# Performance work log

Hardware: AMD Instinct MI355X
Metric: run time of the kernel (lower is better)

## Reference

```python
import jax, jax.numpy as jnp
import numpy as np

TOP_K = 2
SCALE = 1.0  # score_scale_factor

def setup_inputs() -> dict:
    key = jax.random.key(0)
    ks = jax.random.split(key, 8)
    T, D, E, F = 4096, 1024, 8, 4096
    return {
        "hidden_states": jax.random.normal(ks[0], (T, D), jnp.float32),
        "gw1": jax.random.normal(ks[1], (D, D // 4), jnp.float32) * 0.02,
        "gb1": jnp.zeros((D // 4,), jnp.float32),
        "gw2": jax.random.normal(ks[2], (D // 4, D // 16), jnp.float32) * 0.02,
        "gb2": jnp.zeros((D // 16,), jnp.float32),
        "gw3": jax.random.normal(ks[3], (D // 16, E), jnp.float32) * 0.02,
        "w1": jax.random.normal(ks[4], (E, D, F), jnp.float32) * 0.02,
        "b1": jnp.zeros((E, F), jnp.float32),
        "w2": jax.random.normal(ks[5], (E, F, D), jnp.float32) * 0.02,
        "b2": jnp.zeros((E, D), jnp.float32),
    }

def reference(hidden_states, gw1, gb1, gw2, gb2, gw3, w1, b1, w2, b2):
    h = hidden_states                              # [T, D]
    g = jax.nn.relu(h @ gw1 + gb1)
    g = jax.nn.relu(g @ gw2 + gb2)
    router_logits = g @ gw3                        # [T, E]
    probs = jax.nn.softmax(router_logits.astype(jnp.float32), axis=-1)
    top_w, top_i = jax.lax.top_k(probs, TOP_K)     # [T, k]
    top_w = top_w / jnp.sum(top_w, axis=-1, keepdims=True)
    top_w = top_w.astype(h.dtype)
    T, E = router_logits.shape
    # combine weights: scatter normalized top-k weights into dense [T, E]
    cw = jnp.zeros((T, E), h.dtype).at[jnp.arange(T)[:, None], top_i].add(top_w)
    out = jnp.zeros_like(h)
    for e in range(E):  # small fixed expert count
        y = jax.nn.gelu(h @ w1[e] + b1[e]) @ w2[e] + b2[e]
        out = out + y * (cw[:, e:e + 1] * SCALE)
    return out, router_logits
```

## Files before the change

### kernel.cpp

```cpp
#include <hip/hip_runtime.h>
#include <stdint.h>

#define T_  4096
#define D_  1024
#define E_  8
#define F_  4096
#define H1_ 256
#define H2_ 64
#define SCALE_ 1.0f
#define NROW_ (2 * T_)
#define NT2_ 40

typedef unsigned short ushort_t;
typedef unsigned int   uint32;
typedef __attribute__((ext_vector_type(8))) short  short8;
typedef __attribute__((ext_vector_type(4))) float  f32x4;
typedef __attribute__((ext_vector_type(8))) unsigned short us8;

#define BARRIER() do { asm volatile("" ::: "memory"); __builtin_amdgcn_s_barrier(); asm volatile("" ::: "memory"); } while (0)
#define WAITVM(N) asm volatile("s_waitcnt vmcnt(" #N ")" ::: "memory")

__device__ __forceinline__ ushort_t f2bf(float f) {
  uint32 u = __float_as_uint(f);
  u += 0x7FFFu + ((u >> 16) & 1u);
  return (ushort_t)(u >> 16);
}
__device__ __forceinline__ float gelu_tanh(float x) {
  float u = 0.7978845608028654f * (x + 0.044715f * x * x * x);
  float e = __expf(2.0f * u);
  return 0.5f * x * (1.0f + (1.0f - 2.0f / (e + 1.0f)));
}
__device__ __forceinline__ void gll16(const void* gptr, void* lptr) {
  void* g = const_cast<void*>(gptr);
  __builtin_amdgcn_global_load_lds((__attribute__((address_space(1))) void*)g,
                                   (__attribute__((address_space(3))) void*)lptr,
                                   16, 0, 0);
}

__device__ __forceinline__ void stage8(const ushort_t* a0, const ushort_t* a1,
                                       const ushort_t* b0, const ushort_t* b1,
                                       short8 (*An)[16][64], short8 (*Bn)[16][64], int w) {
  gll16(a0,      &An[0][w * 2 + 0][0]);
  gll16(a0 + 32, &An[1][w * 2 + 0][0]);
  gll16(a1,      &An[0][w * 2 + 1][0]);
  gll16(a1 + 32, &An[1][w * 2 + 1][0]);
  gll16(b0,      &Bn[0][w * 2 + 0][0]);
  gll16(b0 + 32, &Bn[1][w * 2 + 0][0]);
  gll16(b1,      &Bn[0][w * 2 + 1][0]);
  gll16(b1 + 32, &Bn[1][w * 2 + 1][0]);
}

__device__ __forceinline__ void mfma_step64(const short8 (*Ac)[16][64], const short8 (*Bc)[16][64],
                                            int wr, int wc, int lane, f32x4 acc[8][4]) {
#pragma unroll
  for (int ks = 0; ks < 2; ++ks) {
    short8 af[8], bf4[4];
#pragma unroll
    for (int i = 0; i < 8; ++i) af[i] = Ac[ks][wr * 8 + i][lane];
#pragma unroll
    for (int j = 0; j < 4; ++j) bf4[j] = Bc[ks][wc * 4 + j][lane];
#pragma unroll
    for (int i = 0; i < 8; ++i)
#pragma unroll
      for (int j = 0; j < 4; ++j)
        acc[i][j] = __builtin_amdgcn_mfma_f32_16x16x32_bf16(af[i], bf4[j], acc[i][j], 0, 0, 0);
  }
}

__global__ void k_cvt_h(const float* __restrict__ h, ushort_t* __restrict__ hb) {
  int i = (blockIdx.x * 256 + threadIdx.x) * 8;
  float4 a = *(const float4*)(h + i);
  float4 b = *(const float4*)(h + i + 4);
  short8 v;
  v[0] = (short)f2bf(a.x); v[1] = (short)f2bf(a.y);
  v[2] = (short)f2bf(a.z); v[3] = (short)f2bf(a.w);
  v[4] = (short)f2bf(b.x); v[5] = (short)f2bf(b.y);
  v[6] = (short)f2bf(b.z); v[7] = (short)f2bf(b.w);
  *(short8*)(hb + i) = v;
}

__global__ void k_transpose_bf16(const float* __restrict__ in, ushort_t* __restrict__ out,
                                 int R, int C) {
  __shared__ float ltf[64][65];
  const size_t per = (size_t)R * C;
  const float* src = in + per * blockIdx.z;
  ushort_t* dst = out + per * blockIdx.z;
  int r0 = blockIdx.x * 64, c0 = blockIdx.y * 64;
  int tid = threadIdx.x;
  int cg = (tid & 15) * 4;
  int rr = tid >> 4;
#pragma unroll
  for (int rb = 0; rb < 64; rb += 16) {
    int r = rb + rr;
    float4 v = *(const float4*)(src + (size_t)(r0 + r) * C + c0 + cg);
    ltf[r][cg + 0] = v.x; ltf[r][cg + 1] = v.y;
    ltf[r][cg + 2] = v.z; ltf[r][cg + 3] = v.w;
  }
  __syncthreads();
  int c = tid >> 2, rch = (tid & 3) * 16;
  ushort_t tmp[16];
#pragma unroll
  for (int i = 0; i < 16; ++i) tmp[i] = f2bf(ltf[rch + i][c]);
  ushort_t* dp = dst + (size_t)(c0 + c) * R + r0 + rch;
  *(us8*)dp = *(const us8*)&tmp[0];
  *(us8*)(dp + 8) = *(const us8*)&tmp[8];
}

__global__ void k_router1(const float* __restrict__ h, const float* __restrict__ gw1,
                          double* __restrict__ p1) {
  __shared__ float sA[16][65];
  __shared__ float sB[16][65];
  int tx = threadIdx.x, ty = threadIdx.y;
  int tid = ty * 16 + tx;
  int m0 = blockIdx.y * 64, n0 = blockIdx.x * 64;
  int kc = blockIdx.z;
  double acc[4][4] = {};
  for (int k0 = kc * 256; k0 < kc * 256 + 256; k0 += 16) {
    {
      int m = tid & 63, kq = tid >> 6;
      float4 v = *(const float4*)(h + (size_t)(m0 + m) * D_ + k0 + kq * 4);
      sA[kq*4+0][m] = v.x; sA[kq*4+1][m] = v.y; sA[kq*4+2][m] = v.z; sA[kq*4+3][m] = v.w;
    }
    {
      int k = tid >> 4, nq = tid & 15;
      float4 v = *(const float4*)(gw1 + (size_t)(k0 + k) * H1_ + n0 + nq * 4);
      sB[k][nq*4+0] = v.x; sB[k][nq*4+1] = v.y; sB[k][nq*4+2] = v.z; sB[k][nq*4+3] = v.w;
    }
    __syncthreads();
#pragma unroll
    for (int k = 0; k < 16; ++k) {
      float a[4], b[4];
#pragma unroll
      for (int i = 0; i < 4; ++i) a[i] = sA[k][ty + i * 16];
#pragma unroll
      for (int j = 0; j < 4; ++j) b[j] = sB[k][tx * 4 + j];
#pragma unroll
      for (int i = 0; i < 4; ++i)
#pragma unroll
        for (int j = 0; j < 4; ++j)
          acc[i][j] += (double)a[i] * (double)b[j];
    }
    __syncthreads();
  }
  double* pd = p1 + (size_t)kc * T_ * H1_;
  for (int i = 0; i < 4; ++i)
    for (int j = 0; j < 4; ++j) {
      int m = m0 + ty + i * 16, n = n0 + tx * 4 + j;
      pd[(size_t)m * H1_ + n] = acc[i][j];
    }
}

__global__ void k_router23(const double* __restrict__ p1, const float* __restrict__ gb1,
                           const float* __restrict__ gw2, const float* __restrict__ gb2,
                           const float* __restrict__ gw3,
                           float* __restrict__ logits_out, int* __restrict__ tokExp,
                           float* __restrict__ tokW, int* __restrict__ counts) {
  __shared__ double sG1[4][256];
  __shared__ double sG2[4][64];
  __shared__ double sL[4][8];
  int lane = threadIdx.x & 63, wv = threadIdx.x >> 6;
  int t = blockIdx.x * 4 + wv;
  const size_t TH = (size_t)T_ * H1_;
  const double* gp = p1 + (size_t)t * H1_ + lane * 4;
  double s0 = 0, s1 = 0, s2 = 0, s3 = 0;
#pragma unroll
  for (int kc = 0; kc < 4; ++kc) {
    double2 va = *(const double2*)(gp + kc * TH);
    double2 vb = *(const double2*)(gp + kc * TH + 2);
    s0 += va.x; s1 += va.y; s2 += vb.x; s3 += vb.y;
  }
  int hbase = lane * 4;
  s0 += (double)gb1[hbase + 0]; s1 += (double)gb1[hbase + 1];
  s2 += (double)gb1[hbase + 2]; s3 += (double)gb1[hbase + 3];
  sG1[wv][hbase + 0] = s0 > 0.0 ? s0 : 0.0;
  sG1[wv][hbase + 1] = s1 > 0.0 ? s1 : 0.0;
  sG1[wv][hbase + 2] = s2 > 0.0 ? s2 : 0.0;
  sG1[wv][hbase + 3] = s3 > 0.0 ? s3 : 0.0;
  __syncthreads();
  double acc = (double)gb2[lane];
  for (int k = 0; k < H1_; ++k)
    acc += sG1[wv][k] * (double)gw2[k * H2_ + lane];
  sG2[wv][lane] = acc > 0.0 ? acc : 0.0;
  __syncthreads();
  if (lane < 8) {
    double l = 0.0;
    for (int j = 0; j < H2_; ++j) l += sG2[wv][j] * (double)gw3[j * E_ + lane];
    sL[wv][lane] = l;
    logits_out[(size_t)t * E_ + lane] = (float)l;
  }
  __syncthreads();
  if (lane == 0) {
    double best = -1e300, second = -1e300; int bi = 0, si = 0;
    for (int e = 0; e < E_; ++e) {
      double l = sL[wv][e];
      if (l > best)        { second = best; si = bi; best = l; bi = e; }
      else if (l > second) { second = l; si = e; }
    }
    double w0 = 1.0 / (1.0 + exp(second - best));
    tokExp[t*2]   = bi; tokExp[t*2+1] = si;
    tokW[t*2]     = (float)w0;
    tokW[t*2+1]   = (float)(1.0 - w0);
    atomicAdd(&counts[bi], 1);
    atomicAdd(&counts[si], 1);
  }
}

__global__ void k_assign(const int* __restrict__ tokExp, const int* __restrict__ counts,
                         int* cursor, int* __restrict__ list, int* __restrict__ rowOf,
                         int* __restrict__ tileTab) {
  int offs[E_];
  int s = 0;
#pragma unroll
  for (int e = 0; e < E_; ++e) { offs[e] = s; s += counts[e]; }
  if (blockIdx.x == 0 && threadIdx.x == 0) {
    int nt = 0;
    for (int e = 0; e < E_; ++e) {
      int cnt = counts[e];
      for (int m = 0; m * 256 < cnt; ++m) {
        tileTab[nt*3+0] = e;
        tileTab[nt*3+1] = offs[e] + m * 256;
        tileTab[nt*3+2] = (cnt - m * 256) < 256 ? (cnt - m * 256) : 256;
        ++nt;
      }
    }
    for (; nt < NT2_; ++nt) tileTab[nt*3+0] = -1;
  }
  int t = blockIdx.x * 256 + threadIdx.x;
  for (int k = 0; k < 2; ++k) {
    int e = tokExp[t*2+k];
    int pos = atomicAdd(&cursor[e], 1);
    int row = offs[e] + pos;
    list[row] = t;
    rowOf[t*2+k] = row;
  }
}

__global__ __launch_bounds__(512, 1) void k_moe_ffn1(
    const ushort_t* __restrict__ hb, const ushort_t* __restrict__ w1t,
    const float* __restrict__ b1, ushort_t* __restrict__ act,
    const int* __restrict__ list, const int* __restrict__ tileTab, int* q) {
  __shared__ short8 lA[2][2][16][64];
  __shared__ short8 lB[2][2][16][64];
  __shared__ int sIdx;
  int tid = threadIdx.x, w = tid >> 6, lane = tid & 63;
  int m16 = lane & 15, kq = lane >> 4;
  int wr = w >> 2, wc = w & 3;
  int quad = lane >> 4, cn = lane & 15;
  for (;;) {
    __syncthreads();
    if (tid == 0) sIdx = atomicAdd(q, 1);
    __syncthreads();
    int idx = sIdx;
    if (idx >= NT2_ * 16) return;
    int ti = idx >> 4, nb = idx & 15;
    int e = tileTab[ti*3+0];
    if (e < 0) continue;
    int rowStart = tileTab[ti*3+1];
    int cntTile  = tileTab[ti*3+2];
    int nBase = nb * 256;
    const ushort_t* B = w1t + (size_t)e * F_ * D_;
    int gr0 = rowStart + w * 32 + m16;
    int gr1 = gr0 + 16;
    int t0 = list[min(gr0, NROW_ - 1)];
    int t1 = list[min(gr1, NROW_ - 1)];
    const ushort_t* aS0 = hb + (size_t)t0 * D_ + kq * 8;
    const ushort_t* aS1 = hb + (size_t)t1 * D_ + kq * 8;
    const ushort_t* bS0 = B + (size_t)(nBase + w * 32 + m16) * D_ + kq * 8;
    const ushort_t* bS1 = bS0 + (size_t)16 * D_;
    f32x4 acc[8][4] = {};
    stage8(aS0, aS1, bS0, bS1, lA[0], lB[0], w);
    const int NSTEP = D_ / 64;
    for (int t = 0; t < NSTEP - 1; ++t) {
      int k0 = (t + 1) * 64;
      stage8(aS0 + k0, aS1 + k0, bS0 + k0, bS1 + k0, lA[(t + 1) & 1], lB[(t + 1) & 1], w);
      WAITVM(8);
      BARRIER();
      mfma_step64(lA[t & 1], lB[t & 1], wr, wc, lane, acc);
      BARRIER();
    }
    WAITVM(0);
    BARRIER();
    mfma_step64(lA[(NSTEP - 1) & 1], lB[(NSTEP - 1) & 1], wr, wc, lane, acc);
    const float* b1e = b1 + (size_t)e * F_;
    float bj[4];
#pragma unroll
    for (int j = 0; j < 4; ++j) bj[j] = b1e[nBase + wc * 64 + j * 16 + cn];
#pragma unroll
    for (int i = 0; i < 8; ++i) {
      int lrow = wr * 128 + i * 16 + quad * 4;
#pragma unroll
      for (int r = 0; r < 4; ++r) {
        if (lrow + r < cntTile) {
          size_t gr = (size_t)rowStart + lrow + r;
#pragma unroll
          for (int j = 0; j < 4; ++j) {
            int n = nBase + wc * 64 + j * 16 + cn;
            float x = acc[i][j][r] + bj[j];
            act[gr * F_ + n] = f2bf(gelu_tanh(x));
          }
        }
      }
    }
  }
}

__global__ __launch_bounds__(512, 1) void k_moe_ffn2(
    const ushort_t* __restrict__ act, const ushort_t* __restrict__ w2t,
    float* __restrict__ part, const int* __restrict__ tileTab, int* q, int KC) {
  __shared__ short8 lA[2][2][16][64];
  __shared__ short8 lB[2][2][16][64];
  __shared__ int sIdx;
  int tid = threadIdx.x, w = tid >> 6, lane = tid & 63;
  int m16 = lane & 15, kq = lane >> 4;
  int wr = w >> 2, wc = w & 3;
  int quad = lane >> 4, cn = lane & 15;
  const int ipt = 4 * KC;
  const int kcs = F_ / KC;
  const int NSTEP = kcs / 64;
  for (;;) {
    __syncthreads();
    if (tid == 0) sIdx = atomicAdd(q, 1);
    __syncthreads();
    int idx = sIdx;
    if (idx >= NT2_ * ipt) return;
    int ti = idx / ipt, sub = idx - ti * ipt;
    int nb = sub / KC, kc = sub - nb * KC;
    int e = tileTab[ti*3+0];
    if (e < 0) continue;
    int rowStart = tileTab[ti*3+1];
    int cntTile  = tileTab[ti*3+2];
    int nBase = nb * 256;
    int kBase = kc * kcs;
    const ushort_t* Bw = w2t + (size_t)e * D_ * F_;
    int gr0 = rowStart + w * 32 + m16;
    int gr1 = gr0 + 16;
    const ushort_t* aS0 = act + (size_t)min(gr0, NROW_ - 1) * F_ + kBase + kq * 8;
    const ushort_t* aS1 = act + (size_t)min(gr1, NROW_ - 1) * F_ + kBase + kq * 8;
    const ushort_t* bS0 = Bw + (size_t)(nBase + w * 32 + m16) * F_ + kBase + kq * 8;
    const ushort_t* bS1 = bS0 + (size_t)16 * F_;
    f32x4 acc[8][4] = {};
    stage8(aS0, aS1, bS0, bS1, lA[0], lB[0], w);
    for (int t = 0; t < NSTEP - 1; ++t) {
      int k0 = (t + 1) * 64;
      stage8(aS0 + k0, aS1 + k0, bS0 + k0, bS1 + k0, lA[(t + 1) & 1], lB[(t + 1) & 1], w);
      WAITVM(8);
      BARRIER();
      mfma_step64(lA[t & 1], lB[t & 1], wr, wc, lane, acc);
      BARRIER();
    }
    WAITVM(0);
    BARRIER();
    mfma_step64(lA[(NSTEP - 1) & 1], lB[(NSTEP - 1) & 1], wr, wc, lane, acc);
    float* pd = part + (size_t)kc * NROW_ * D_;
#pragma unroll
    for (int i = 0; i < 8; ++i) {
      int lrow = wr * 128 + i * 16 + quad * 4;
#pragma unroll
      for (int r = 0; r < 4; ++r) {
        if (lrow + r < cntTile) {
          size_t gr = (size_t)rowStart + lrow + r;
#pragma unroll
          for (int j = 0; j < 4; ++j) {
            int n = nBase + wc * 64 + j * 16 + cn;
            pd[gr * D_ + n] = acc[i][j][r];
          }
        }
      }
    }
  }
}

__global__ void k_combine(const float* __restrict__ part, const int* __restrict__ rowOf,
                          const int* __restrict__ tokExp, const float* __restrict__ tokW,
                          const float* __restrict__ b2, float* __restrict__ out, int KC) {
  int t = blockIdx.x;
  int rA = rowOf[t*2], rB = rowOf[t*2+1];
  int eA = tokExp[t*2], eB = tokExp[t*2+1];
  float wA = tokW[t*2] * SCALE_, wB = tokW[t*2+1] * SCALE_;
  int d = threadIdx.x * 4;
  const size_t P = (size_t)NROW_ * D_;
  float sax = 0, say = 0, saz = 0, saw = 0;
  float sbx = 0, sby = 0, sbz = 0, sbw = 0;
  for (int k = 0; k < KC; ++k) {
    float4 a = *(const float4*)(part + (size_t)k * P + (size_t)rA * D_ + d);
    float4 b = *(const float4*)(part + (size_t)k * P + (size_t)rB * D_ + d);
    sax += a.x; say += a.y; saz += a.z; saw += a.w;
    sbx += b.x; sby += b.y; sbz += b.z; sbw += b.w;
  }
  float4 ba = *(const float4*)(b2 + (size_t)eA * D_ + d);
  float4 bb = *(const float4*)(b2 + (size_t)eB * D_ + d);
  float4 o;
  o.x = wA * (sax + ba.x) + wB * (sbx + bb.x);
  o.y = wA * (say + ba.y) + wB * (sby + bb.y);
  o.z = wA * (saz + ba.z) + wB * (sbz + bb.z);
  o.w = wA * (saw + ba.w) + wB * (sbw + bb.w);
  *(float4*)(out + (size_t)t * D_ + d) = o;
}

extern "C" void kernel_launch(void* const* d_in, const int* in_sizes, int n_in,
                              void* d_out, int out_size, void* d_ws, size_t ws_size,
                              hipStream_t stream) {
  const float* h   = (const float*)d_in[0];
  const float* gw1 = (const float*)d_in[1];
  const float* gb1 = (const float*)d_in[2];
  const float* gw2 = (const float*)d_in[3];
  const float* gb2 = (const float*)d_in[4];
  const float* gw3 = (const float*)d_in[5];
  const float* w1  = (const float*)d_in[6];
  const float* b1  = (const float*)d_in[7];
  const float* w2  = (const float*)d_in[8];
  const float* b2  = (const float*)d_in[9];
  float* out    = (float*)d_out;
  float* logits = out + (size_t)T_ * D_;

  char* ws = (char*)d_ws;
  size_t o = 0;
  auto alloc = [&](size_t bytes) -> void* {
    o = (o + 255) & ~(size_t)255;
    void* p = ws + o;
    o += bytes;
    return p;
  };
  int*      counts  = (int*)alloc((2 * E_ + 2) * 4);
  int*      cursor  = counts + E_;
  int*      qq      = counts + 2 * E_;
  int*      tileTab = (int*)alloc((size_t)NT2_ * 3 * 4);
  int*      tokExp  = (int*)alloc((size_t)T_ * 2 * 4);
  float*    tokW    = (float*)alloc((size_t)T_ * 2 * 4);
  int*      list    = (int*)alloc((size_t)NROW_ * 4);
  int*      rowOf   = (int*)alloc((size_t)NROW_ * 4);
  ushort_t* hb      = (ushort_t*)alloc((size_t)T_ * D_ * 2);
  ushort_t* w2t     = (ushort_t*)alloc((size_t)E_ * D_ * F_ * 2);
  char*     bigA    = (char*)alloc((size_t)NROW_ * F_ * 2);
  double*   p1      = (double*)bigA;
  ushort_t* act     = (ushort_t*)bigA;
  size_t oAligned = (o + 255) & ~(size_t)255;
  size_t w1tBytes = (size_t)E_ * D_ * F_ * 2;
  int KC = (ws_size >= oAligned + (size_t)4 * NROW_ * D_ * 4) ? 4 : 2;
  size_t partBytes = (size_t)KC * NROW_ * D_ * 4;
  char*     bigB    = (char*)alloc(partBytes > w1tBytes ? partBytes : w1tBytes);
  ushort_t* w1t     = (ushort_t*)bigB;
  float*    part    = (float*)bigB;
  (void)in_sizes; (void)n_in; (void)out_size;

  hipMemsetAsync(counts, 0, (2 * E_ + 2) * 4, stream);
  k_cvt_h<<<T_ * D_ / 2048, 256, 0, stream>>>(h, hb);
  k_transpose_bf16<<<dim3(D_ / 64, F_ / 64, E_), 256, 0, stream>>>(w1, w1t, D_, F_);
  k_transpose_bf16<<<dim3(F_ / 64, D_ / 64, E_), 256, 0, stream>>>(w2, w2t, F_, D_);
  k_router1<<<dim3(H1_ / 64, T_ / 64, 4), dim3(16, 16), 0, stream>>>(h, gw1, p1);
  k_router23<<<T_ / 4, 256, 0, stream>>>(p1, gb1, gw2, gb2, gw3, logits, tokExp, tokW, counts);
  k_assign<<<T_ / 256, 256, 0, stream>>>(tokExp, counts, cursor, list, rowOf, tileTab);
  k_moe_ffn1<<<256, 512, 0, stream>>>(hb, w1t, b1, act, list, tileTab, qq + 0);
  k_moe_ffn2<<<256, 512, 0, stream>>>(act, w2t, part, tileTab, qq + 1, KC);
  k_combine<<<T_, 256, 0, stream>>>(part, rowOf, tokExp, tokW, b2, out, KC);
}
```

Baseline: 906.9 us.

## Shrink FFN GEMM tiles to 256x128 and use three-stage LDS pipeline

Both expert GEMM kernels change from 256x256 output tiles to 256x128, with a 4x2 wave grid in place of 2x4, and per-wave accumulators halve. The double-buffered LDS loop with two barriers per k-step becomes a triple-buffered ring with one barrier per step, so loads run two steps ahead of the MFMA work. The aim is more work items for load balance, lower register pressure and better latency hiding. The cost is less reuse of each A tile, since every row block is now loaded twice as often per output column.

```diff
diff --git a/kernel.cpp b/kernel.cpp
--- a/kernel.cpp
+++ b/kernel.cpp
@@ -37,30 +37,28 @@
                                    16, 0, 0);
 }
 
-__device__ __forceinline__ void stage8(const ushort_t* a0, const ushort_t* a1,
-                                       const ushort_t* b0, const ushort_t* b1,
-                                       short8 (*An)[16][64], short8 (*Bn)[16][64], int w) {
+__device__ __forceinline__ void stage6(const ushort_t* a0, const ushort_t* a1,
+                                       const ushort_t* b0,
+                                       short8 (*An)[16][64], short8 (*Bn)[8][64], int w) {
   gll16(a0,      &An[0][w * 2 + 0][0]);
   gll16(a0 + 32, &An[1][w * 2 + 0][0]);
   gll16(a1,      &An[0][w * 2 + 1][0]);
   gll16(a1 + 32, &An[1][w * 2 + 1][0]);
-  gll16(b0,      &Bn[0][w * 2 + 0][0]);
-  gll16(b0 + 32, &Bn[1][w * 2 + 0][0]);
-  gll16(b1,      &Bn[0][w * 2 + 1][0]);
-  gll16(b1 + 32, &Bn[1][w * 2 + 1][0]);
-}
-
-__device__ __forceinline__ void mfma_step64(const short8 (*Ac)[16][64], const short8 (*Bc)[16][64],
-                                            int wr, int wc, int lane, f32x4 acc[8][4]) {
+  gll16(b0,      &Bn[0][w][0]);
+  gll16(b0 + 32, &Bn[1][w][0]);
+}
+
+__device__ __forceinline__ void mfma_step32(const short8 (*Ac)[16][64], const short8 (*Bc)[8][64],
+                                            int wr, int wc, int lane, f32x4 acc[4][4]) {
 #pragma unroll
   for (int ks = 0; ks < 2; ++ks) {
-    short8 af[8], bf4[4];
-#pragma unroll
-    for (int i = 0; i < 8; ++i) af[i] = Ac[ks][wr * 8 + i][lane];
+    short8 af[4], bf4[4];
+#pragma unroll
+    for (int i = 0; i < 4; ++i) af[i] = Ac[ks][wr * 4 + i][lane];
 #pragma unroll
     for (int j = 0; j < 4; ++j) bf4[j] = Bc[ks][wc * 4 + j][lane];
 #pragma unroll
-    for (int i = 0; i < 8; ++i)
+    for (int i = 0; i < 4; ++i)
 #pragma unroll
       for (int j = 0; j < 4; ++j)
         acc[i][j] = __builtin_amdgcn_mfma_f32_16x16x32_bf16(af[i], bf4[j], acc[i][j], 0, 0, 0);
@@ -239,25 +237,25 @@
     const ushort_t* __restrict__ hb, const ushort_t* __restrict__ w1t,
     const float* __restrict__ b1, ushort_t* __restrict__ act,
     const int* __restrict__ list, const int* __restrict__ tileTab, int* q) {
-  __shared__ short8 lA[2][2][16][64];
-  __shared__ short8 lB[2][2][16][64];
+  __shared__ short8 lA[3][2][16][64];
+  __shared__ short8 lB[3][2][8][64];
   __shared__ int sIdx;
   int tid = threadIdx.x, w = tid >> 6, lane = tid & 63;
   int m16 = lane & 15, kq = lane >> 4;
-  int wr = w >> 2, wc = w & 3;
+  int wr = w >> 1, wc = w & 1;
   int quad = lane >> 4, cn = lane & 15;
   for (;;) {
     __syncthreads();
     if (tid == 0) sIdx = atomicAdd(q, 1);
     __syncthreads();
     int idx = sIdx;
-    if (idx >= NT2_ * 16) return;
-    int ti = idx >> 4, nb = idx & 15;
+    if (idx >= NT2_ * 32) return;
+    int ti = idx >> 5, nb = idx & 31;
     int e = tileTab[ti*3+0];
     if (e < 0) continue;
     int rowStart = tileTab[ti*3+1];
     int cntTile  = tileTab[ti*3+2];
-    int nBase = nb * 256;
+    int nBase = nb * 128;
     const ushort_t* B = w1t + (size_t)e * F_ * D_;
     int gr0 = rowStart + w * 32 + m16;
     int gr1 = gr0 + 16;
@@ -265,29 +263,31 @@
     int t1 = list[min(gr1, NROW_ - 1)];
     const ushort_t* aS0 = hb + (size_t)t0 * D_ + kq * 8;
     const ushort_t* aS1 = hb + (size_t)t1 * D_ + kq * 8;
-    const ushort_t* bS0 = B + (size_t)(nBase + w * 32 + m16) * D_ + kq * 8;
-    const ushort_t* bS1 = bS0 + (size_t)16 * D_;
-    f32x4 acc[8][4] = {};
-    stage8(aS0, aS1, bS0, bS1, lA[0], lB[0], w);
+    const ushort_t* bS0 = B + (size_t)(nBase + w * 16 + m16) * D_ + kq * 8;
+    f32x4 acc[4][4] = {};
+    short8 (*A0)[16][64] = lA[0], (*A1)[16][64] = lA[1], (*A2)[16][64] = lA[2];
+    short8 (*B0)[8][64] = lB[0], (*B1)[8][64] = lB[1], (*B2)[8][64] = lB[2];
+    stage6(aS0, aS1, bS0, A0, B0, w);
+    stage6(aS0 + 64, aS1 + 64, bS0 + 64, A1, B1, w);
     const int NSTEP = D_ / 64;
-    for (int t = 0; t < NSTEP - 1; ++t) {
-      int k0 = (t + 1) * 64;
-      stage8(aS0 + k0, aS1 + k0, bS0 + k0, bS1 + k0, lA[(t + 1) & 1], lB[(t + 1) & 1], w);
-      WAITVM(8);
+    for (int t = 0; t < NSTEP - 2; ++t) {
+      WAITVM(6);
       BARRIER();
-      mfma_step64(lA[t & 1], lB[t & 1], wr, wc, lane, acc);
-      BARRIER();
-    }
-    WAITVM(0);
-    BARRIER();
-    mfma_step64(lA[(NSTEP - 1) & 1], lB[(NSTEP - 1) & 1], wr, wc, lane, acc);
+      int k0 = (t + 2) * 64;
+      stage6(aS0 + k0, aS1 + k0, bS0 + k0, A2, B2, w);
+      mfma_step32(A0, B0, wr, wc, lane, acc);
+      short8 (*ta)[16][64] = A0; A0 = A1; A1 = A2; A2 = ta;
+      short8 (*tb)[8][64]  = B0; B0 = B1; B1 = B2; B2 = tb;
+    }
+    WAITVM(6); BARRIER(); mfma_step32(A0, B0, wr, wc, lane, acc);
+    WAITVM(0); BARRIER(); mfma_step32(A1, B1, wr, wc, lane, acc);
     const float* b1e = b1 + (size_t)e * F_;
     float bj[4];
 #pragma unroll
     for (int j = 0; j < 4; ++j) bj[j] = b1e[nBase + wc * 64 + j * 16 + cn];
 #pragma unroll
-    for (int i = 0; i < 8; ++i) {
-      int lrow = wr * 128 + i * 16 + quad * 4;
+    for (int i = 0; i < 4; ++i) {
+      int lrow = wr * 64 + i * 16 + quad * 4;
 #pragma unroll
       for (int r = 0; r < 4; ++r) {
         if (lrow + r < cntTile) {
@@ -307,14 +307,14 @@
 __global__ __launch_bounds__(512, 1) void k_moe_ffn2(
     const ushort_t* __restrict__ act, const ushort_t* __restrict__ w2t,
     float* __restrict__ part, const int* __restrict__ tileTab, int* q, int KC) {
-  __shared__ short8 lA[2][2][16][64];
-  __shared__ short8 lB[2][2][16][64];
+  __shared__ short8 lA[3][2][16][64];
+  __shared__ short8 lB[3][2][8][64];
   __shared__ int sIdx;
   int tid = threadIdx.x, w = tid >> 6, lane = tid & 63;
   int m16 = lane & 15, kq = lane >> 4;
-  int wr = w >> 2, wc = w & 3;
+  int wr = w >> 1, wc = w & 1;
   int quad = lane >> 4, cn = lane & 15;
-  const int ipt = 4 * KC;
+  const int ipt = 8 * KC;
   const int kcs = F_ / KC;
   const int NSTEP = kcs / 64;
   for (;;) {
@@ -329,32 +329,34 @@
     if (e < 0) continue;
     int rowStart = tileTab[ti*3+1];
     int cntTile  = tileTab[ti*3+2];
-    int nBase = nb * 256;
+    int nBase = nb * 128;
     int kBase = kc * kcs;
     const ushort_t* Bw = w2t + (size_t)e * D_ * F_;
     int gr0 = rowStart + w * 32 + m16;
     int gr1 = gr0 + 16;
     const ushort_t* aS0 = act + (size_t)min(gr0, NROW_ - 1) * F_ + kBase + kq * 8;
     const ushort_t* aS1 = act + (size_t)min(gr1, NROW_ - 1) * F_ + kBase + kq * 8;
-    const ushort_t* bS0 = Bw + (size_t)(nBase + w * 32 + m16) * F_ + kBase + kq * 8;
-    const ushort_t* bS1 = bS0 + (size_t)16 * F_;
-    f32x4 acc[8][4] = {};
-    stage8(aS0, aS1, bS0, bS1, lA[0], lB[0], w);
-    for (int t = 0; t < NSTEP - 1; ++t) {
-      int k0 = (t + 1) * 64;
-      stage8(aS0 + k0, aS1 + k0, bS0 + k0, bS1 + k0, lA[(t + 1) & 1], lB[(t + 1) & 1], w);
-      WAITVM(8);
+    const ushort_t* bS0 = Bw + (size_t)(nBase + w * 16 + m16) * F_ + kBase + kq * 8;
+    f32x4 acc[4][4] = {};
+    short8 (*A0)[16][64] = lA[0], (*A1)[16][64] = lA[1], (*A2)[16][64] = lA[2];
+    short8 (*B0)[8][64] = lB[0], (*B1)[8][64] = lB[1], (*B2)[8][64] = lB[2];
+    stage6(aS0, aS1, bS0, A0, B0, w);
+    stage6(aS0 + 64, aS1 + 64, bS0 + 64, A1, B1, w);
+    for (int t = 0; t < NSTEP - 2; ++t) {
+      WAITVM(6);
       BARRIER();
-      mfma_step64(lA[t & 1], lB[t & 1], wr, wc, lane, acc);
-      BARRIER();
-    }
-    WAITVM(0);
-    BARRIER();
-    mfma_step64(lA[(NSTEP - 1) & 1], lB[(NSTEP - 1) & 1], wr, wc, lane, acc);
+      int k0 = (t + 2) * 64;
+      stage6(aS0 + k0, aS1 + k0, bS0 + k0, A2, B2, w);
+      mfma_step32(A0, B0, wr, wc, lane, acc);
+      short8 (*ta)[16][64] = A0; A0 = A1; A1 = A2; A2 = ta;
+      short8 (*tb)[8][64]  = B0; B0 = B1; B1 = B2; B2 = tb;
+    }
+    WAITVM(6); BARRIER(); mfma_step32(A0, B0, wr, wc, lane, acc);
+    WAITVM(0); BARRIER(); mfma_step32(A1, B1, wr, wc, lane, acc);
     float* pd = part + (size_t)kc * NROW_ * D_;
 #pragma unroll
-    for (int i = 0; i < 8; ++i) {
-      int lrow = wr * 128 + i * 16 + quad * 4;
+    for (int i = 0; i < 4; ++i) {
+      int lrow = wr * 64 + i * 16 + quad * 4;
 #pragma unroll
       for (int r = 0; r < 4; ++r) {
         if (lrow + r < cntTile) {
```

After: 964.6 us. 1.06x slower.
